# Kernel optimization log

Hardware: AMD Instinct MI355X
Metric: run time of the kernel (lower is better)

## Reference

```python
import jax, jax.numpy as jnp
import numpy as np

D_MODEL = 1024
NHEAD = 16
D_K = D_MODEL // NHEAD


def setup_inputs() -> dict:
    key = jax.random.key(0)
    ks = jax.random.split(key, 9)
    s = 1.0 / np.sqrt(D_MODEL)
    return {
        "x": jax.random.normal(ks[0], (4, 2048, D_MODEL), dtype=jnp.float32),
        "Wq": jax.random.uniform(ks[1], (D_MODEL, D_MODEL), jnp.float32, -s, s),
        "bq": jax.random.uniform(ks[2], (D_MODEL,), jnp.float32, -s, s),
        "Wk": jax.random.uniform(ks[3], (D_MODEL, D_MODEL), jnp.float32, -s, s),
        "bk": jax.random.uniform(ks[4], (D_MODEL,), jnp.float32, -s, s),
        "Wv": jax.random.uniform(ks[5], (D_MODEL, D_MODEL), jnp.float32, -s, s),
        "bv": jax.random.uniform(ks[6], (D_MODEL,), jnp.float32, -s, s),
        "Wo": jax.random.uniform(ks[7], (D_MODEL, D_MODEL), jnp.float32, -s, s),
        "bo": jax.random.uniform(ks[8], (D_MODEL,), jnp.float32, -s, s),
    }


def reference(x, Wq, bq, Wk, bk, Wv, bv, Wo, bo):
    B, S, D = x.shape
    H, dk = NHEAD, D_K

    def split_heads(t):  # [B,S,D] -> [B,H,S,dk]
        return t.reshape(B, S, H, dk).transpose(0, 2, 1, 3)

    q = split_heads(x @ Wq + bq)
    k = split_heads(x @ Wk + bk)
    v = split_heads(x @ Wv + bv)

    scores = jnp.einsum('bhqd,bhkd->bhqk', q, k) / jnp.sqrt(jnp.float32(dk))
    attn = jax.nn.softmax(scores, axis=-1)
    out = jnp.einsum('bhqk,bhkd->bhqd', attn, v)  # [B,H,S,dk]
    out = out.transpose(0, 2, 1, 3).reshape(B, S, D)
    return out @ Wo + bo
```

## Files before the change

kernel.cpp:

```cpp
#include <hip/hip_runtime.h>


typedef short short8 __attribute__((ext_vector_type(8)));
typedef float f32x4 __attribute__((ext_vector_type(4)));
typedef float f32x16 __attribute__((ext_vector_type(16)));

#define DMODEL 1024
#define NH 16
#define DK 64
#define SEQ 2048
#define NB 4
#define MTOT (NB*SEQ)
#define KSCALE 0.18033688f

__device__ __forceinline__ unsigned short f2bf(float f) {
    union { float f; unsigned u; } v; v.f = f;
    unsigned r = (v.u + 0x7FFFu + ((v.u >> 16) & 1u)) >> 16;
    return (unsigned short)r;
}

__device__ __forceinline__ unsigned pk2(float a, float b) {
    unsigned r;
    asm("v_cvt_pk_bf16_f32 %0, %1, %2" : "=v"(r) : "v"(a), "v"(b));
    return r;
}

__device__ __forceinline__ float exp2a(float x) {
    float r; asm("v_exp_f32 %0, %1" : "=v"(r) : "v"(x)); return r;
}

__device__ __forceinline__ float max3a(float a, float b, float c) {
    float r; asm("v_max3_f32 %0, %1, %2, %3" : "=v"(r) : "v"(a), "v"(b), "v"(c)); return r;
}

__device__ __forceinline__ void plswap(unsigned &a, unsigned &b) {
    asm volatile("v_permlane32_swap_b32 %0, %1" : "+v"(a), "+v"(b));
}

__device__ __forceinline__ void gload16(const short* g, short* l) {
    __builtin_amdgcn_global_load_lds(
        (const __attribute__((address_space(1))) unsigned*)(const void*)g,
        (__attribute__((address_space(3))) unsigned*)(void*)l,
        16, 0, 0);
}

union Frag { short8 s8; unsigned u[4]; };

__global__ __launch_bounds__(256) void cvt_kernel(const float* __restrict__ in,
                                                  short* __restrict__ out, int n4) {
    int i = blockIdx.x * 256 + threadIdx.x;
    if (i >= n4) return;
    float4 v = ((const float4*)in)[i];
    short4 o;
    o.x = (short)f2bf(v.x); o.y = (short)f2bf(v.y);
    o.z = (short)f2bf(v.z); o.w = (short)f2bf(v.w);
    ((short4*)out)[i] = o;
}

__global__ __launch_bounds__(256) void transpose_kernel(const float* __restrict__ W,
                                                        short* __restrict__ Wt) {
    __shared__ float t[32][33];
    int r0 = blockIdx.y * 32, c0 = blockIdx.x * 32;
    int tr = threadIdx.x >> 3;
    int tc = (threadIdx.x & 7) * 4;
    float4 v = *(const float4*)&W[(r0 + tr) * DMODEL + c0 + tc];
    t[tr][tc + 0] = v.x; t[tr][tc + 1] = v.y; t[tr][tc + 2] = v.z; t[tr][tc + 3] = v.w;
    __syncthreads();
    short4 o;
    o.x = (short)f2bf(t[tc + 0][tr]);
    o.y = (short)f2bf(t[tc + 1][tr]);
    o.z = (short)f2bf(t[tc + 2][tr]);
    o.w = (short)f2bf(t[tc + 3][tr]);
    *(short4*)&Wt[(c0 + tr) * DMODEL + r0 + tc] = o;
}

template<int MODE>
__global__ __launch_bounds__(256) void gemm_kernel(
    const short* __restrict__ A, const short* __restrict__ Bt,
    const float* __restrict__ b0, const float* __restrict__ b1, const float* __restrict__ b2,
    short* __restrict__ Qb, short* __restrict__ Kb, short* __restrict__ Vtb,
    float* __restrict__ Cout)
{
    __shared__ __align__(16) short As[128 * 64];
    __shared__ __align__(16) short Bs[128 * 64];
    const int K = DMODEL;
    int m0 = blockIdx.y * 128, n0 = blockIdx.x * 128;
    int tid = threadIdx.x, lane = tid & 63, wid = tid >> 6;
    int wm = (wid >> 1) * 64, wn = (wid & 1) * 64;

    int srow = 8 * wid + (lane >> 3);
    int scol = ((lane & 7) ^ (lane >> 3)) * 8;
    const short* aSrc = A + (size_t)(m0 + srow) * K + scol;
    const short* bSrc = Bt + (size_t)(n0 + srow) * K + scol;

    f32x4 acc[4][4];
    #pragma unroll
    for (int i = 0; i < 4; i++)
        #pragma unroll
        for (int j = 0; j < 4; j++) acc[i][j] = (f32x4){0.f, 0.f, 0.f, 0.f};

    for (int kt = 0; kt < K; kt += 64) {
        #pragma unroll
        for (int i = 0; i < 4; ++i) {
            gload16(aSrc + (size_t)(32 * i) * K + kt, &As[(8 * wid + 32 * i) * 64]);
            gload16(bSrc + (size_t)(32 * i) * K + kt, &Bs[(8 * wid + 32 * i) * 64]);
        }
        __syncthreads();
        #pragma unroll
        for (int kk = 0; kk < 2; ++kk) {
            int ko = kk * 32 + (lane >> 4) * 8;
            short8 af[4], bfv[4];
            #pragma unroll
            for (int i = 0; i < 4; i++) {
                int r = wm + i * 16 + (lane & 15);
                af[i] = *(const short8*)&As[(r * 64 + ko) ^ ((r & 7) << 3)];
            }
            #pragma unroll
            for (int j = 0; j < 4; j++) {
                int r = wn + j * 16 + (lane & 15);
                bfv[j] = *(const short8*)&Bs[(r * 64 + ko) ^ ((r & 7) << 3)];
            }
            #pragma unroll
            for (int i = 0; i < 4; i++)
                #pragma unroll
                for (int j = 0; j < 4; j++)
                    acc[i][j] = __builtin_amdgcn_mfma_f32_16x16x32_bf16(af[i], bfv[j], acc[i][j], 0, 0, 0);
        }
        __syncthreads();
    }

    #pragma unroll
    for (int i = 0; i < 4; i++) {
        #pragma unroll
        for (int j = 0; j < 4; j++) {
            int col = n0 + wn + j * 16 + (lane & 15);
            #pragma unroll
            for (int r = 0; r < 4; r++) {
                int row = m0 + wm + i * 16 + (lane >> 4) * 4 + r;
                float v = acc[i][j][r];
                if (MODE == 0) {
                    int seg = col >> 10, c = col & 1023;
                    const float* bp = (seg == 0) ? b0 : (seg == 1 ? b1 : b2);
                    v += bp[c];
                    if (seg == 1) v *= KSCALE;
                    unsigned short bv = f2bf(v);
                    int hh = c >> 6, d = c & 63, bb = row >> 11, s = row & 2047;
                    if (seg == 0)      Qb [(((bb * NH + hh) * SEQ) + s) * DK + d] = (short)bv;
                    else if (seg == 1) Kb [(((bb * NH + hh) * SEQ) + s) * DK + d] = (short)bv;
                    else               Vtb[(((bb * NH + hh) * DK) + d) * SEQ + s] = (short)bv;
                } else {
                    Cout[row * DMODEL + col] = v + b0[col];
                }
            }
        }
    }
}

__global__ __launch_bounds__(256) void attn_kernel(
    const short* __restrict__ Qb, const short* __restrict__ Kb,
    const short* __restrict__ Vtb, short* __restrict__ AOb)
{
    __shared__ __align__(16) short Ks[64 * 64];
    __shared__ __align__(16) short Vs[64 * 64];
    char* ksb = (char*)Ks;
    char* vsb = (char*)Vs;

    int bid = blockIdx.x;
    int wk = (bid & 7) * 128 + (bid >> 3);
    int qi = wk & 15, bh = wk >> 4;
    int h = bh & (NH - 1), b = bh >> 4;
    int q0 = qi * 128;

    int tid = threadIdx.x, lane = tid & 63, wid = tid >> 6;
    int hi = lane >> 5, l31 = lane & 31, l7 = lane & 7;
    const short* Qp = Qb + (size_t)bh * SEQ * DK;
    const short* Kp = Kb + (size_t)bh * SEQ * DK;
    const short* Vp = Vtb + (size_t)bh * DK * SEQ;

    short8 qf[4];
    #pragma unroll
    for (int ks = 0; ks < 4; ks++)
        qf[ks] = *(const short8*)&Qp[(q0 + wid * 32 + l31) * DK + ks * 16 + hi * 8];

    f32x16 ot0, ot1;
    #pragma unroll
    for (int r = 0; r < 16; r++) { ot0[r] = 0.f; ot1[r] = 0.f; }
    float mrun = -1e30f, lrun = 0.f;

    int srow = tid >> 3, ssl = tid & 7;
    #pragma unroll
    for (int i = 0; i < 2; i++) {
        int row = srow + 32 * i;
        *(short8*)(ksb + ((row * 128 + ssl * 16) ^ ((row & 7) << 4))) =
            *(const short8*)&Kp[row * DK + ssl * 8];
        *(short8*)(vsb + ((row * 128 + ssl * 16) ^ ((row & 7) << 4))) =
            *(const short8*)&Vp[row * SEQ + ssl * 8];
    }
    __syncthreads();

    const int NT = SEQ / 64;
    for (int t = 0; t < NT; ++t) {
        short8 nk[2], nv[2];
        if (t + 1 < NT) {
            int kv0n = (t + 1) * 64;
            #pragma unroll
            for (int i = 0; i < 2; i++) {
                int row = srow + 32 * i;
                nk[i] = *(const short8*)&Kp[(kv0n + row) * DK + ssl * 8];
                nv[i] = *(const short8*)&Vp[row * SEQ + kv0n + ssl * 8];
            }
        }

        f32x16 st0, st1;
        #pragma unroll
        for (int r = 0; r < 16; r++) { st0[r] = 0.f; st1[r] = 0.f; }
        __builtin_amdgcn_s_setprio(1);
        #pragma unroll
        for (int ks = 0; ks < 4; ks++) {
            short8 kf0 = *(const short8*)(ksb + ((l31 * 128 + ks * 32 + hi * 16) ^ (l7 << 4)));
            short8 kf1 = *(const short8*)(ksb + (((32 + l31) * 128 + ks * 32 + hi * 16) ^ (l7 << 4)));
            st0 = __builtin_amdgcn_mfma_f32_32x32x16_bf16(kf0, qf[ks], st0, 0, 0, 0);
            st1 = __builtin_amdgcn_mfma_f32_32x32x16_bf16(kf1, qf[ks], st1, 0, 0, 0);
        }
        __builtin_amdgcn_s_setprio(0);

        float m8[8];
        #pragma unroll
        for (int i = 0; i < 8; i++) m8[i] = max3a(st0[i], st0[i + 8], st1[i]);
        float m4[4];
        #pragma unroll
        for (int i = 0; i < 4; i++) m4[i] = max3a(m8[i], m8[i + 4], st1[i + 8]);
        float m2a = max3a(m4[0], m4[2], st1[12]);
        float m2b = max3a(m4[1], m4[3], st1[13]);
        float mxv = max3a(m2a, m2b, st1[14]);
        mxv = fmaxf(mxv, st1[15]);
        float mt = fmaxf(mxv, __shfl_xor(mxv, 32, 64));

        if (!__all(mt - mrun <= 11.0f)) {
            float mn = fmaxf(mrun, mt);
            float al = exp2a(mrun - mn);
            lrun *= al;
            #pragma unroll
            for (int r = 0; r < 16; r++) { ot0[r] *= al; ot1[r] *= al; }
            mrun = mn;
        }
        #pragma unroll
        for (int r = 0; r < 16; r++) {
            st0[r] = exp2a(st0[r] - mrun);
            st1[r] = exp2a(st1[r] - mrun);
        }
        float s16[16];
        #pragma unroll
        for (int r = 0; r < 16; r++) s16[r] = st0[r] + st1[r];
        #pragma unroll
        for (int s = 8; s > 0; s >>= 1)
            #pragma unroll
            for (int r = 0; r < 8; r++) if (r < s) s16[r] += s16[r + s];
        lrun += s16[0] + __shfl_xor(s16[0], 32, 64);

        unsigned w0[8], w1[8];
        #pragma unroll
        for (int m = 0; m < 4; m++) {
            w0[m * 2]     = pk2(st0[4 * m], st0[4 * m + 1]);
            w0[m * 2 + 1] = pk2(st0[4 * m + 2], st0[4 * m + 3]);
            w1[m * 2]     = pk2(st1[4 * m], st1[4 * m + 1]);
            w1[m * 2 + 1] = pk2(st1[4 * m + 2], st1[4 * m + 3]);
        }
        short8 pf[4];
        #pragma unroll
        for (int ks = 0; ks < 4; ks++) {
            unsigned a0 = (ks < 2) ? w0[4 * (ks & 1) + 0] : w1[4 * (ks & 1) + 0];
            unsigned b0_ = (ks < 2) ? w0[4 * (ks & 1) + 2] : w1[4 * (ks & 1) + 2];
            unsigned a1 = (ks < 2) ? w0[4 * (ks & 1) + 1] : w1[4 * (ks & 1) + 1];
            unsigned b1_ = (ks < 2) ? w0[4 * (ks & 1) + 3] : w1[4 * (ks & 1) + 3];
            plswap(a0, b0_);
            plswap(a1, b1_);
            Frag f;
            f.u[0] = a0; f.u[1] = a1; f.u[2] = b0_; f.u[3] = b1_;
            pf[ks] = f.s8;
        }

        __builtin_amdgcn_s_setprio(1);
        #pragma unroll
        for (int ks = 0; ks < 4; ks++) {
            short8 vf0 = *(const short8*)(vsb + ((l31 * 128 + ks * 32 + hi * 16) ^ (l7 << 4)));
            short8 vf1 = *(const short8*)(vsb + (((32 + l31) * 128 + ks * 32 + hi * 16) ^ (l7 << 4)));
            ot0 = __builtin_amdgcn_mfma_f32_32x32x16_bf16(vf0, pf[ks], ot0, 0, 0, 0);
            ot1 = __builtin_amdgcn_mfma_f32_32x32x16_bf16(vf1, pf[ks], ot1, 0, 0, 0);
        }
        __builtin_amdgcn_s_setprio(0);

        __syncthreads();
        if (t + 1 < NT) {
            #pragma unroll
            for (int i = 0; i < 2; i++) {
                int row = srow + 32 * i;
                *(short8*)(ksb + ((row * 128 + ssl * 16) ^ ((row & 7) << 4))) = nk[i];
                *(short8*)(vsb + ((row * 128 + ssl * 16) ^ ((row & 7) << 4))) = nv[i];
            }
        }
        __syncthreads();
    }

    float inv = 1.f / lrun;
    int srow_q = b * SEQ + q0 + wid * 32 + l31;
    short* outp = AOb + (size_t)srow_q * DMODEL + h * DK;
    #pragma unroll
    for (int g = 0; g < 4; g++) {
        int d0 = 8 * g + 4 * hi;
        uint2 u;
        u.x = pk2(ot0[4 * g] * inv, ot0[4 * g + 1] * inv);
        u.y = pk2(ot0[4 * g + 2] * inv, ot0[4 * g + 3] * inv);
        *(uint2*)&outp[d0] = u;
        uint2 v2;
        v2.x = pk2(ot1[4 * g] * inv, ot1[4 * g + 1] * inv);
        v2.y = pk2(ot1[4 * g + 2] * inv, ot1[4 * g + 3] * inv);
        *(uint2*)&outp[32 + d0] = v2;
    }
}

extern "C" void kernel_launch(void* const* d_in, const int* in_sizes, int n_in,
                              void* d_out, int out_size, void* d_ws, size_t ws_size,
                              hipStream_t stream)
{
    const float* x  = (const float*)d_in[0];
    const float* Wq = (const float*)d_in[1];
    const float* bq = (const float*)d_in[2];
    const float* Wk = (const float*)d_in[3];
    const float* bk = (const float*)d_in[4];
    const float* Wv = (const float*)d_in[5];
    const float* bv = (const float*)d_in[6];
    const float* Wo = (const float*)d_in[7];
    const float* bo = (const float*)d_in[8];
    float* out = (float*)d_out;

    char* w = (char*)d_ws;
    short* xb    = (short*)w; w += (size_t)MTOT * DMODEL * 2;
    short* Wqkvt = (short*)w; w += (size_t)3 * DMODEL * DMODEL * 2;
    short* Wot   = (short*)w; w += (size_t)DMODEL * DMODEL * 2;
    short* Qb    = (short*)w; w += (size_t)MTOT * DMODEL * 2;
    short* Kb    = (short*)w; w += (size_t)MTOT * DMODEL * 2;
    short* Vtb   = (short*)w; w += (size_t)MTOT * DMODEL * 2;
    short* AOb   = (short*)w; w += (size_t)MTOT * DMODEL * 2;

    cvt_kernel<<<(MTOT * DMODEL / 4 + 255) / 256, 256, 0, stream>>>(x, xb, MTOT * DMODEL / 4);

    dim3 tg(32, 32);
    transpose_kernel<<<tg, 256, 0, stream>>>(Wq, Wqkvt);
    transpose_kernel<<<tg, 256, 0, stream>>>(Wk, Wqkvt + DMODEL * DMODEL);
    transpose_kernel<<<tg, 256, 0, stream>>>(Wv, Wqkvt + 2 * DMODEL * DMODEL);
    transpose_kernel<<<tg, 256, 0, stream>>>(Wo, Wot);

    gemm_kernel<0><<<dim3(3 * DMODEL / 128, MTOT / 128), 256, 0, stream>>>(
        xb, Wqkvt, bq, bk, bv, Qb, Kb, Vtb, nullptr);

    attn_kernel<<<dim3(SEQ / 128 * NH * NB), 256, 0, stream>>>(Qb, Kb, Vtb, AOb);

    gemm_kernel<1><<<dim3(DMODEL / 128, MTOT / 128), 256, 0, stream>>>(
        AOb, Wot, bo, nullptr, nullptr, nullptr, nullptr, nullptr, out);
}
```

Measured before the change: 226.3 us.

## Double-buffer GEMM LDS with half-K stages and fuse prep kernels

Rewrites the bf16 GEMM main loop to use a double-buffered LDS layout split into 32-wide K halves. Global-to-LDS loads for upcoming stages are issued before the MFMAs of the current stage, with explicit vmcnt/lgkmcnt waits, raw barriers and s_setprio to overlap memory with compute. It also merges the x conversion and the four weight-transpose launches into one prep kernel to cut launch overhead. The cost is more complex wait-count logic that has to match exactly the number of outstanding loads, and a new swizzle pattern for the 32-wide LDS rows.

```diff
diff --git a/kernel.cpp b/kernel.cpp
--- a/kernel.cpp
+++ b/kernel.cpp
@@ -44,23 +44,36 @@
         16, 0, 0);
 }
 
+__device__ __forceinline__ void vm8()   { asm volatile("s_waitcnt vmcnt(8)"   ::: "memory"); }
+__device__ __forceinline__ void vm4()   { asm volatile("s_waitcnt vmcnt(4)"   ::: "memory"); }
+__device__ __forceinline__ void vm0()   { asm volatile("s_waitcnt vmcnt(0)"   ::: "memory"); }
+__device__ __forceinline__ void lgkm0() { asm volatile("s_waitcnt lgkmcnt(0)" ::: "memory"); }
+
 union Frag { short8 s8; unsigned u[4]; };
 
-__global__ __launch_bounds__(256) void cvt_kernel(const float* __restrict__ in,
-                                                  short* __restrict__ out, int n4) {
-    int i = blockIdx.x * 256 + threadIdx.x;
-    if (i >= n4) return;
-    float4 v = ((const float4*)in)[i];
-    short4 o;
-    o.x = (short)f2bf(v.x); o.y = (short)f2bf(v.y);
-    o.z = (short)f2bf(v.z); o.w = (short)f2bf(v.w);
-    ((short4*)out)[i] = o;
-}
-
-__global__ __launch_bounds__(256) void transpose_kernel(const float* __restrict__ W,
-                                                        short* __restrict__ Wt) {
+#define NCVT (MTOT * DMODEL / 4 / 256)
+__global__ __launch_bounds__(256) void prep_kernel(
+    const float* __restrict__ x, short* __restrict__ xb,
+    const float* __restrict__ Wq, const float* __restrict__ Wk,
+    const float* __restrict__ Wv, const float* __restrict__ Wo,
+    short* __restrict__ Wqkvt, short* __restrict__ Wot)
+{
     __shared__ float t[32][33];
-    int r0 = blockIdx.y * 32, c0 = blockIdx.x * 32;
+    int bid = blockIdx.x;
+    if (bid < NCVT) {
+        int i = bid * 256 + threadIdx.x;
+        float4 v = ((const float4*)x)[i];
+        short4 o;
+        o.x = (short)f2bf(v.x); o.y = (short)f2bf(v.y);
+        o.z = (short)f2bf(v.z); o.w = (short)f2bf(v.w);
+        ((short4*)xb)[i] = o;
+        return;
+    }
+    int wb = bid - NCVT;
+    int widx = wb >> 10, tile = wb & 1023;
+    const float* W = (widx == 0) ? Wq : (widx == 1) ? Wk : (widx == 2) ? Wv : Wo;
+    short* dst = (widx < 3) ? (Wqkvt + (size_t)widx * DMODEL * DMODEL) : Wot;
+    int r0 = (tile >> 5) * 32, c0 = (tile & 31) * 32;
     int tr = threadIdx.x >> 3;
     int tc = (threadIdx.x & 7) * 4;
     float4 v = *(const float4*)&W[(r0 + tr) * DMODEL + c0 + tc];
@@ -71,7 +84,7 @@
     o.y = (short)f2bf(t[tc + 1][tr]);
     o.z = (short)f2bf(t[tc + 2][tr]);
     o.w = (short)f2bf(t[tc + 3][tr]);
-    *(short4*)&Wt[(c0 + tr) * DMODEL + r0 + tc] = o;
+    *(short4*)&dst[(c0 + tr) * DMODEL + r0 + tc] = o;
 }
 
 template<int MODE>
@@ -81,17 +94,17 @@
     short* __restrict__ Qb, short* __restrict__ Kb, short* __restrict__ Vtb,
     float* __restrict__ Cout)
 {
-    __shared__ __align__(16) short As[128 * 64];
-    __shared__ __align__(16) short Bs[128 * 64];
+    __shared__ __align__(16) short L[2][2][2][128 * 32];
     const int K = DMODEL;
+    const int NKT = K / 64;
     int m0 = blockIdx.y * 128, n0 = blockIdx.x * 128;
     int tid = threadIdx.x, lane = tid & 63, wid = tid >> 6;
     int wm = (wid >> 1) * 64, wn = (wid & 1) * 64;
 
-    int srow = 8 * wid + (lane >> 3);
-    int scol = ((lane & 7) ^ (lane >> 3)) * 8;
-    const short* aSrc = A + (size_t)(m0 + srow) * K + scol;
-    const short* bSrc = Bt + (size_t)(n0 + srow) * K + scol;
+    int srowl = (lane >> 2);
+    int scoll = ((lane & 3) ^ ((lane >> 3) & 3)) * 8;
+    const short* aSrc = A + (size_t)(m0 + wid * 32 + srowl) * K + scoll;
+    const short* bSrc = Bt + (size_t)(n0 + wid * 32 + srowl) * K + scoll;
 
     f32x4 acc[4][4];
     #pragma unroll
@@ -99,34 +112,73 @@
         #pragma unroll
         for (int j = 0; j < 4; j++) acc[i][j] = (f32x4){0.f, 0.f, 0.f, 0.f};
 
-    for (int kt = 0; kt < K; kt += 64) {
-        #pragma unroll
-        for (int i = 0; i < 4; ++i) {
-            gload16(aSrc + (size_t)(32 * i) * K + kt, &As[(8 * wid + 32 * i) * 64]);
-            gload16(bSrc + (size_t)(32 * i) * K + kt, &Bs[(8 * wid + 32 * i) * 64]);
-        }
-        __syncthreads();
-        #pragma unroll
-        for (int kk = 0; kk < 2; ++kk) {
-            int ko = kk * 32 + (lane >> 4) * 8;
+    auto STAGE = [&](int kt, int kkh) {
+        int buf = kt & 1;
+        const short* as = aSrc + (size_t)kt * 64 + kkh * 32;
+        const short* bs = bSrc + (size_t)kt * 64 + kkh * 32;
+        #pragma unroll
+        for (int i = 0; i < 2; ++i) {
+            gload16(as + (size_t)i * 16 * K, &L[buf][0][kkh][(wid * 32 + i * 16) * 32]);
+            gload16(bs + (size_t)i * 16 * K, &L[buf][1][kkh][(wid * 32 + i * 16) * 32]);
+        }
+    };
+    auto LDA = [&](int buf, int kkh, short8* f) {
+        #pragma unroll
+        for (int m = 0; m < 4; m++) {
+            int r = wm + m * 16 + (lane & 15);
+            f[m] = *(const short8*)&L[buf][0][kkh][r * 32 + (((lane >> 4) ^ ((r >> 1) & 3)) * 8)];
+        }
+    };
+    auto LDB = [&](int buf, int kkh, short8* f) {
+        #pragma unroll
+        for (int n = 0; n < 4; n++) {
+            int r = wn + n * 16 + (lane & 15);
+            f[n] = *(const short8*)&L[buf][1][kkh][r * 32 + (((lane >> 4) ^ ((r >> 1) & 3)) * 8)];
+        }
+    };
+
+    STAGE(0, 0);
+    STAGE(0, 1);
+    STAGE(1, 0);
+    vm8();
+    __builtin_amdgcn_s_barrier();
+
+    for (int k = 0; k < NKT; ++k) {
+        int buf = k & 1;
+        {
             short8 af[4], bfv[4];
-            #pragma unroll
-            for (int i = 0; i < 4; i++) {
-                int r = wm + i * 16 + (lane & 15);
-                af[i] = *(const short8*)&As[(r * 64 + ko) ^ ((r & 7) << 3)];
-            }
-            #pragma unroll
-            for (int j = 0; j < 4; j++) {
-                int r = wn + j * 16 + (lane & 15);
-                bfv[j] = *(const short8*)&Bs[(r * 64 + ko) ^ ((r & 7) << 3)];
-            }
+            LDA(buf, 0, af); LDB(buf, 0, bfv);
+            if (k + 1 < NKT) STAGE(k + 1, 1);
+            lgkm0();
+            __builtin_amdgcn_s_barrier();
+            __builtin_amdgcn_s_setprio(1);
             #pragma unroll
             for (int i = 0; i < 4; i++)
                 #pragma unroll
                 for (int j = 0; j < 4; j++)
                     acc[i][j] = __builtin_amdgcn_mfma_f32_16x16x32_bf16(af[i], bfv[j], acc[i][j], 0, 0, 0);
-        }
-        __syncthreads();
+            __builtin_amdgcn_s_setprio(0);
+            if (k == NKT - 1) vm0(); else vm8();
+            __builtin_amdgcn_s_barrier();
+        }
+        {
+            short8 af[4], bfv[4];
+            LDA(buf, 1, af); LDB(buf, 1, bfv);
+            if (k + 2 < NKT) STAGE(k + 2, 0);
+            lgkm0();
+            __builtin_amdgcn_s_barrier();
+            __builtin_amdgcn_s_setprio(1);
+            #pragma unroll
+            for (int i = 0; i < 4; i++)
+                #pragma unroll
+                for (int j = 0; j < 4; j++)
+                    acc[i][j] = __builtin_amdgcn_mfma_f32_16x16x32_bf16(af[i], bfv[j], acc[i][j], 0, 0, 0);
+            __builtin_amdgcn_s_setprio(0);
+            if (k < NKT - 1) {
+                if (k == NKT - 2) vm4(); else vm8();
+                __builtin_amdgcn_s_barrier();
+            }
+        }
     }
 
     #pragma unroll
@@ -343,13 +395,7 @@
     short* Vtb   = (short*)w; w += (size_t)MTOT * DMODEL * 2;
     short* AOb   = (short*)w; w += (size_t)MTOT * DMODEL * 2;
 
-    cvt_kernel<<<(MTOT * DMODEL / 4 + 255) / 256, 256, 0, stream>>>(x, xb, MTOT * DMODEL / 4);
-
-    dim3 tg(32, 32);
-    transpose_kernel<<<tg, 256, 0, stream>>>(Wq, Wqkvt);
-    transpose_kernel<<<tg, 256, 0, stream>>>(Wk, Wqkvt + DMODEL * DMODEL);
-    transpose_kernel<<<tg, 256, 0, stream>>>(Wv, Wqkvt + 2 * DMODEL * DMODEL);
-    transpose_kernel<<<tg, 256, 0, stream>>>(Wo, Wot);
+    prep_kernel<<<NCVT + 4096, 256, 0, stream>>>(x, xb, Wq, Wk, Wv, Wo, Wqkvt, Wot);
 
     gemm_kernel<0><<<dim3(3 * DMODEL / 128, MTOT / 128), 256, 0, stream>>>(
         xb, Wqkvt, bq, bk, bv, Qb, Kb, Vtb, nullptr);
```

After: 222.6 us. About the same (-1.6%).
